# Kernel optimization log

Measured on AMD Instinct MI355X. Metric: run time of the kernel, lower is better.

The kernel has to match this reference:

```python
import jax, jax.numpy as jnp
import numpy as np

NUM_HEADS = 16
MASK_NEG = -66504.0  # matches IPEX causal mask fill value


def setup_inputs() -> dict:
    key = jax.random.key(0)
    ks = jax.random.split(key, 5)
    B, S, E = 1, 2048, 2048
    return {
        "hidden_states": jax.random.normal(ks[0], (B, S, E), dtype=jnp.float32),
        "q_wei": jax.random.normal(ks[1], (E, E), dtype=jnp.float32) * (E ** -0.5),
        "k_wei": jax.random.normal(ks[2], (E, E), dtype=jnp.float32) * (E ** -0.5),
        "v_wei": jax.random.normal(ks[3], (E, E), dtype=jnp.float32) * (E ** -0.5),
        "out_wei": jax.random.normal(ks[4], (E, E), dtype=jnp.float32) * (E ** -0.5),
    }


def reference(hidden_states, q_wei, k_wei, v_wei, out_wei):
    B, S, E = hidden_states.shape
    H = NUM_HEADS
    D = E // H
    # qkv_normal (row-major path): x @ W, [B,S,E]
    q = hidden_states @ q_wei
    k = hidden_states @ k_wei
    v = hidden_states @ v_wei
    # compute_qkv view + normal_combine permute -> [B,H,S,D]
    q = q.reshape(B, S, H, D).transpose(0, 2, 1, 3)
    k = k.reshape(B, S, H, D).transpose(0, 2, 1, 3)
    v = v.reshape(B, S, H, D).transpose(0, 2, 1, 3)
    # naive_self_attention: scores, causal mask add, THEN scale divide
    scores = jnp.einsum("bhqd,bhkd->bhqk", q, k)  # [B,H,S,S]
    causal = jnp.triu(jnp.full((S, S), MASK_NEG, dtype=scores.dtype), k=1)
    scores = scores + causal[None, None]
    scores = scores / jnp.sqrt(jnp.asarray(D, dtype=scores.dtype))
    probs = jax.nn.softmax(scores.astype(jnp.float32), axis=-1).astype(q.dtype)
    attn = jnp.einsum("bhqk,bhkd->bhqd", probs, v)  # [B,H,S,D]
    # merge heads and output projection
    attn = attn.transpose(0, 2, 1, 3).reshape(B, S, E)
    return attn @ out_wei
```

## Files before the change

kernel.cpp:

```cpp
#include <hip/hip_runtime.h>

#define F16 _Float16
typedef __attribute__((ext_vector_type(8))) _Float16 half8;
typedef __attribute__((ext_vector_type(4))) float f32x4;

constexpr int S = 2048;
constexpr int E = 2048;
constexpr float MASK_NEG = -66504.0f;
constexpr float INV_SQRT_D = 0.08838834764831845f;
constexpr float MASK_SC = MASK_NEG * INV_SQRT_D;

__device__ __forceinline__ void gload16(const void* g, void* l) {
  __builtin_amdgcn_global_load_lds((const __attribute__((address_space(1))) void*)g,
                                   (__attribute__((address_space(3))) void*)l, 16, 0, 0);
}

__global__ __launch_bounds__(256) void cast_f32_f16_k(const float* __restrict__ x,
                                                      F16* __restrict__ y) {
  size_t i = ((size_t)blockIdx.x * 256 + threadIdx.x) * 8;
  float4 a = *(const float4*)(x + i);
  float4 b = *(const float4*)(x + i + 4);
  half8 h;
  h[0] = (F16)a.x; h[1] = (F16)a.y; h[2] = (F16)a.z; h[3] = (F16)a.w;
  h[4] = (F16)b.x; h[5] = (F16)b.y; h[6] = (F16)b.z; h[7] = (F16)b.w;
  *(half8*)(y + i) = h;
}

__global__ __launch_bounds__(256) void transpose_cast2_k(const float* __restrict__ W0,
                                                         const float* __restrict__ W1,
                                                         F16* __restrict__ D0,
                                                         F16* __restrict__ D1) {
  const float* W = blockIdx.z ? W1 : W0;
  F16* Wt = blockIdx.z ? D1 : D0;
  __shared__ float tile[64][65];
  const int t = threadIdx.x;
  const int bx = blockIdx.x, by = blockIdx.y;
  {
    int r = t >> 4, c = (t & 15) << 2;
    const float* src = W + (size_t)(by * 64 + r) * E + bx * 64 + c;
    #pragma unroll
    for (int i = 0; i < 4; ++i) {
      float4 v = *(const float4*)(src + (size_t)i * 16 * E);
      tile[r + i * 16][c + 0] = v.x; tile[r + i * 16][c + 1] = v.y;
      tile[r + i * 16][c + 2] = v.z; tile[r + i * 16][c + 3] = v.w;
    }
  }
  __syncthreads();
  {
    int r = t >> 2, c = (t & 3) << 4;
    half8 v0, v1;
    #pragma unroll
    for (int i = 0; i < 8; ++i) v0[i] = (F16)tile[c + i][r];
    #pragma unroll
    for (int i = 0; i < 8; ++i) v1[i] = (F16)tile[c + 8 + i][r];
    F16* dst = Wt + (size_t)(bx * 64 + r) * E + by * 64 + c;
    *(half8*)dst = v0;
    *(half8*)(dst + 8) = v1;
  }
}

template <int MODE>
__global__ __launch_bounds__(256, 2) void gemm_bt_k(const F16* __restrict__ A,
                                                    const F16* __restrict__ Bt,
                                                    void* __restrict__ C0v,
                                                    void* __restrict__ C1v) {
  constexpr int K = 2048, N = 2048;
  __shared__ F16 sA[128 * 64];
  __shared__ F16 sB[128 * 64];
  const int t = threadIdx.x;
  const int lane = t & 63, wave = t >> 6;
  const int wr = wave >> 1, wc = wave & 1;
  const int bm = blockIdx.y, bn = blockIdx.x;

  f32x4 acc[4][4];
  #pragma unroll
  for (int mi = 0; mi < 4; ++mi)
    #pragma unroll
    for (int ni = 0; ni < 4; ++ni) acc[mi][ni] = (f32x4){0.f, 0.f, 0.f, 0.f};

  const int rb = t >> 3;
  const int bofs = (t & 7) << 4;
  const int kOff = (bofs ^ ((rb & 7) << 4)) >> 1;
  const F16* aSrc = A + (size_t)(bm * 128 + rb) * K + kOff;
  const F16* bSrc = Bt + (size_t)(bn * 128 + rb) * K + kOff;
  F16* aDst = sA + t * 8;
  F16* bDst = sB + t * 8;

  for (int bk = 0; bk < K; bk += 64) {
    #pragma unroll
    for (int it = 0; it < 4; ++it) {
      gload16(aSrc + (size_t)it * 32 * K + bk, aDst + it * 2048);
      gload16(bSrc + (size_t)it * 32 * K + bk, bDst + it * 2048);
    }
    __syncthreads();
    #pragma unroll
    for (int kk = 0; kk < 2; ++kk) {
      half8 af[4], bf[4];
      const int kb = kk * 64 + ((lane >> 4) << 4);
      #pragma unroll
      for (int i = 0; i < 4; ++i) {
        const int ra = wr * 64 + i * 16 + (lane & 15);
        af[i] = *(const half8*)((const char*)sA + ra * 128 + (kb ^ ((ra & 7) << 4)));
        const int rn = wc * 64 + i * 16 + (lane & 15);
        bf[i] = *(const half8*)((const char*)sB + rn * 128 + (kb ^ ((rn & 7) << 4)));
      }
      #pragma unroll
      for (int mi = 0; mi < 4; ++mi)
        #pragma unroll
        for (int ni = 0; ni < 4; ++ni)
          acc[mi][ni] = __builtin_amdgcn_mfma_f32_16x16x32_f16(af[mi], bf[ni], acc[mi][ni], 0, 0, 0);
    }
    __syncthreads();
  }

  const float scale = (MODE == 1 && bn < 16) ? INV_SQRT_D : 1.0f;
  void* Cv = (MODE == 1 && bn >= 16) ? C1v : C0v;
  const int cb = (MODE == 1 ? (bn & 15) : bn) * 128;

  #pragma unroll
  for (int mi = 0; mi < 4; ++mi) {
    const int r0 = bm * 128 + wr * 64 + mi * 16 + ((lane >> 4) << 2);
    #pragma unroll
    for (int ni = 0; ni < 4; ++ni) {
      const int c = cb + wc * 64 + ni * 16 + (lane & 15);
      #pragma unroll
      for (int j = 0; j < 4; ++j) {
        if (MODE == 2)
          ((float*)Cv)[(size_t)(r0 + j) * N + c] = acc[mi][ni][j];
        else
          ((F16*)Cv)[(size_t)(r0 + j) * N + c] = (F16)(acc[mi][ni][j] * scale);
      }
    }
  }
}

__global__ __launch_bounds__(256, 2) void attn_fwd_k(const F16* __restrict__ Q,
                                                     const F16* __restrict__ Km,
                                                     const F16* __restrict__ Vt,
                                                     F16* __restrict__ O) {
  __shared__ F16 sK[2][64 * 128];
  __shared__ F16 sV[2][128 * 64];
  __shared__ F16 sP[64 * 64];
  const int t = threadIdx.x, lane = t & 63, w = t >> 6;
  const int h = blockIdx.x & 15, qt = 31 - (blockIdx.x >> 4);
  const int qrow0 = qt * 64 + w * 16;

  half8 qf[4];
  {
    const int r = qrow0 + (lane & 15);
    const F16* qp = Q + (size_t)r * E + h * 128 + ((lane >> 4) << 3);
    #pragma unroll
    for (int kd = 0; kd < 4; ++kd) qf[kd] = *(const half8*)(qp + kd * 32);
  }

  f32x4 oacc[8];
  #pragma unroll
  for (int i = 0; i < 8; ++i) oacc[i] = (f32x4){0.f, 0.f, 0.f, 0.f};
  float mrow[4] = {-3e38f, -3e38f, -3e38f, -3e38f};
  float lrow[4] = {0.f, 0.f, 0.f, 0.f};

  const int rk = t >> 4;
  const int kcol = (((t & 15) << 4) ^ ((rk & 15) << 4)) >> 1;
  const int rv = t >> 3;
  const int vcol = (((t & 7) << 4) ^ ((rv & 7) << 4)) >> 1;
  const F16* kBase = Km + (size_t)rk * E + h * 128 + kcol;
  const F16* vBase = Vt + (size_t)(h * 128 + rv) * S + vcol;

  auto stage = [&](int kt, int b) {
    const F16* kSrc = kBase + (size_t)kt * 64 * E;
    const F16* vSrc = vBase + kt * 64;
    #pragma unroll
    for (int it = 0; it < 4; ++it) {
      gload16(kSrc + (size_t)it * 16 * E, &sK[b][t * 8 + it * 2048]);
      gload16(vSrc + (size_t)it * 32 * S, &sV[b][t * 8 + it * 2048]);
    }
  };

  stage(0, 0);

  for (int kt = 0; kt <= qt; ++kt) {
    __syncthreads();
    if (kt < qt) stage(kt + 1, (kt + 1) & 1);
    const char* bK = (const char*)sK[kt & 1];
    const char* bV = (const char*)sV[kt & 1];

    f32x4 sacc[4];
    #pragma unroll
    for (int i = 0; i < 4; ++i) sacc[i] = (f32x4){0.f, 0.f, 0.f, 0.f};
    #pragma unroll
    for (int kd = 0; kd < 4; ++kd) {
      const int kb = kd * 64 + ((lane >> 4) << 4);
      #pragma unroll
      for (int ni = 0; ni < 4; ++ni) {
        const int rn = ni * 16 + (lane & 15);
        half8 bf = *(const half8*)(bK + rn * 256 + (kb ^ ((rn & 15) << 4)));
        sacc[ni] = __builtin_amdgcn_mfma_f32_16x16x32_f16(qf[kd], bf, sacc[ni], 0, 0, 0);
      }
    }

    const bool diag = (kt == qt);
    float pvv[4][4];
    const int qg0 = qrow0 + ((lane >> 4) << 2);
    const int kg0 = kt * 64 + (lane & 15);
    #pragma unroll
    for (int j = 0; j < 4; ++j) {
      float mx = -3e38f;
      #pragma unroll
      for (int ni = 0; ni < 4; ++ni) {
        float s = sacc[ni][j];
        if (diag && (kg0 + ni * 16) > (qg0 + j)) s += MASK_SC;
        pvv[ni][j] = s;
        mx = fmaxf(mx, s);
      }
      mx = fmaxf(mx, __shfl_xor(mx, 1));
      mx = fmaxf(mx, __shfl_xor(mx, 2));
      mx = fmaxf(mx, __shfl_xor(mx, 4));
      mx = fmaxf(mx, __shfl_xor(mx, 8));
      const float mnew = fmaxf(mrow[j], mx);
      const float sc = __expf(mrow[j] - mnew);
      float rs = 0.f;
      #pragma unroll
      for (int ni = 0; ni < 4; ++ni) {
        const float p = __expf(pvv[ni][j] - mnew);
        pvv[ni][j] = p;
        rs += p;
      }
      rs += __shfl_xor(rs, 1);
      rs += __shfl_xor(rs, 2);
      rs += __shfl_xor(rs, 4);
      rs += __shfl_xor(rs, 8);
      lrow[j] = lrow[j] * sc + rs;
      mrow[j] = mnew;
      #pragma unroll
      for (int df = 0; df < 8; ++df) oacc[df][j] *= sc;
    }

    {
      const int rl0 = w * 16 + ((lane >> 4) << 2);
      #pragma unroll
      for (int ni = 0; ni < 4; ++ni) {
        const int cb = (ni * 16 + (lane & 15)) * 2;
        #pragma unroll
        for (int j = 0; j < 4; ++j) {
          const int r = rl0 + j;
          *(F16*)((char*)sP + r * 128 + (cb ^ ((r & 7) << 4))) = (F16)pvv[ni][j];
        }
      }
    }

    #pragma unroll
    for (int kk = 0; kk < 2; ++kk) {
      const int kb = kk * 64 + ((lane >> 4) << 4);
      const int ra = w * 16 + (lane & 15);
      half8 pa = *(const half8*)((const char*)sP + ra * 128 + (kb ^ ((ra & 7) << 4)));
      #pragma unroll
      for (int df = 0; df < 8; ++df) {
        const int rd = df * 16 + (lane & 15);
        half8 vf = *(const half8*)(bV + rd * 128 + (kb ^ ((rd & 7) << 4)));
        oacc[df] = __builtin_amdgcn_mfma_f32_16x16x32_f16(pa, vf, oacc[df], 0, 0, 0);
      }
    }
  }

  #pragma unroll
  for (int j = 0; j < 4; ++j) {
    const float inv = 1.0f / lrow[j];
    const int r = qrow0 + ((lane >> 4) << 2) + j;
    F16* op = O + (size_t)r * E + h * 128 + (lane & 15);
    #pragma unroll
    for (int df = 0; df < 8; ++df) op[df * 16] = (F16)(oacc[df][j] * inv);
  }
}

extern "C" void kernel_launch(void* const* d_in, const int* in_sizes, int n_in,
                              void* d_out, int out_size, void* d_ws, size_t ws_size,
                              hipStream_t stream) {
  const float* X  = (const float*)d_in[0];
  const float* Wq = (const float*)d_in[1];
  const float* Wk = (const float*)d_in[2];
  const float* Wv = (const float*)d_in[3];
  const float* Wo = (const float*)d_in[4];
  float* out = (float*)d_out;

  const size_t MAT = (size_t)2048 * 2048;
  F16* Xh  = (F16*)d_ws;
  F16* Wt0 = Xh + MAT;
  F16* Wt1 = Wt0 + MAT;
  F16* Qh  = Wt1 + MAT;
  F16* Kh  = Qh + MAT;
  F16* Vh  = Kh + MAT;

  dim3 b256(256);
  cast_f32_f16_k<<<dim3(MAT / 2048), b256, 0, stream>>>(X, Xh);

  transpose_cast2_k<<<dim3(32, 32, 2), b256, 0, stream>>>(Wq, Wk, Wt0, Wt1);
  gemm_bt_k<1><<<dim3(32, 16), b256, 0, stream>>>(Xh, Wt0, Qh, Kh);

  transpose_cast2_k<<<dim3(32, 32, 2), b256, 0, stream>>>(Wv, Wo, Wt0, Wt1);
  gemm_bt_k<0><<<dim3(16, 16), b256, 0, stream>>>(Wt0, Xh, Vh, nullptr);

  attn_fwd_k<<<dim3(512), b256, 0, stream>>>(Qh, Kh, Vh, Xh);

  gemm_bt_k<2><<<dim3(16, 16), b256, 0, stream>>>(Xh, Wt1, out, nullptr);
}
```

Measured before the change: 196.2 us.

## Shrink GEMM M-tile, per-wave P buffers, lazy softmax rescale, priority hints in attention

The GEMM tile height drops from 128 to 64 rows, doubling grid size so the 256-CU part gets more blocks for the 2048x2048 projections, at the cost of lower arithmetic intensity per block. The attention kernel interleaves long and short causal query tiles in block order, gives each wave a private P buffer, and raises wave priority around the MFMA sections. It also skips the running-max rescale of the output accumulator unless a row's max grows by more than a threshold of 8. That trades exact max tracking for fewer exponentials and multiplies, accepting larger but bounded exponent values.

```diff
diff --git a/kernel.cpp b/kernel.cpp
--- a/kernel.cpp
+++ b/kernel.cpp
@@ -65,47 +65,51 @@
                                                     void* __restrict__ C0v,
                                                     void* __restrict__ C1v) {
   constexpr int K = 2048, N = 2048;
-  __shared__ F16 sA[128 * 64];
+  __shared__ F16 sA[64 * 64];
   __shared__ F16 sB[128 * 64];
   const int t = threadIdx.x;
   const int lane = t & 63, wave = t >> 6;
   const int wr = wave >> 1, wc = wave & 1;
   const int bm = blockIdx.y, bn = blockIdx.x;
 
-  f32x4 acc[4][4];
+  f32x4 acc[2][4];
   #pragma unroll
-  for (int mi = 0; mi < 4; ++mi)
+  for (int mi = 0; mi < 2; ++mi)
     #pragma unroll
     for (int ni = 0; ni < 4; ++ni) acc[mi][ni] = (f32x4){0.f, 0.f, 0.f, 0.f};
 
   const int rb = t >> 3;
   const int bofs = (t & 7) << 4;
   const int kOff = (bofs ^ ((rb & 7) << 4)) >> 1;
-  const F16* aSrc = A + (size_t)(bm * 128 + rb) * K + kOff;
+  const F16* aSrc = A + (size_t)(bm * 64 + rb) * K + kOff;
   const F16* bSrc = Bt + (size_t)(bn * 128 + rb) * K + kOff;
   F16* aDst = sA + t * 8;
   F16* bDst = sB + t * 8;
 
   for (int bk = 0; bk < K; bk += 64) {
     #pragma unroll
-    for (int it = 0; it < 4; ++it) {
+    for (int it = 0; it < 2; ++it)
       gload16(aSrc + (size_t)it * 32 * K + bk, aDst + it * 2048);
+    #pragma unroll
+    for (int it = 0; it < 4; ++it)
       gload16(bSrc + (size_t)it * 32 * K + bk, bDst + it * 2048);
-    }
     __syncthreads();
     #pragma unroll
     for (int kk = 0; kk < 2; ++kk) {
-      half8 af[4], bf[4];
+      half8 af[2], bf[4];
       const int kb = kk * 64 + ((lane >> 4) << 4);
       #pragma unroll
+      for (int i = 0; i < 2; ++i) {
+        const int ra = wr * 32 + i * 16 + (lane & 15);
+        af[i] = *(const half8*)((const char*)sA + ra * 128 + (kb ^ ((ra & 7) << 4)));
+      }
+      #pragma unroll
       for (int i = 0; i < 4; ++i) {
-        const int ra = wr * 64 + i * 16 + (lane & 15);
-        af[i] = *(const half8*)((const char*)sA + ra * 128 + (kb ^ ((ra & 7) << 4)));
         const int rn = wc * 64 + i * 16 + (lane & 15);
         bf[i] = *(const half8*)((const char*)sB + rn * 128 + (kb ^ ((rn & 7) << 4)));
       }
       #pragma unroll
-      for (int mi = 0; mi < 4; ++mi)
+      for (int mi = 0; mi < 2; ++mi)
         #pragma unroll
         for (int ni = 0; ni < 4; ++ni)
           acc[mi][ni] = __builtin_amdgcn_mfma_f32_16x16x32_f16(af[mi], bf[ni], acc[mi][ni], 0, 0, 0);
@@ -118,8 +122,8 @@
   const int cb = (MODE == 1 ? (bn & 15) : bn) * 128;
 
   #pragma unroll
-  for (int mi = 0; mi < 4; ++mi) {
-    const int r0 = bm * 128 + wr * 64 + mi * 16 + ((lane >> 4) << 2);
+  for (int mi = 0; mi < 2; ++mi) {
+    const int r0 = bm * 64 + wr * 32 + mi * 16 + ((lane >> 4) << 2);
     #pragma unroll
     for (int ni = 0; ni < 4; ++ni) {
       const int c = cb + wc * 64 + ni * 16 + (lane & 15);
@@ -140,9 +144,11 @@
                                                      F16* __restrict__ O) {
   __shared__ F16 sK[2][64 * 128];
   __shared__ F16 sV[2][128 * 64];
-  __shared__ F16 sP[64 * 64];
+  __shared__ F16 sP[4][16 * 64];
   const int t = threadIdx.x, lane = t & 63, w = t >> 6;
-  const int h = blockIdx.x & 15, qt = 31 - (blockIdx.x >> 4);
+  const int h = blockIdx.x & 15;
+  const int bq = blockIdx.x >> 4;
+  const int qt = (bq < 16) ? (31 - bq) : (bq - 16);
   const int qrow0 = qt * 64 + w * 16;
 
   half8 qf[4];
@@ -165,6 +171,7 @@
   const int vcol = (((t & 7) << 4) ^ ((rv & 7) << 4)) >> 1;
   const F16* kBase = Km + (size_t)rk * E + h * 128 + kcol;
   const F16* vBase = Vt + (size_t)(h * 128 + rv) * S + vcol;
+  F16* myP = (F16*)sP[w];
 
   auto stage = [&](int kt, int b) {
     const F16* kSrc = kBase + (size_t)kt * 64 * E;
@@ -177,16 +184,18 @@
   };
 
   stage(0, 0);
-
-  for (int kt = 0; kt <= qt; ++kt) {
+  const int nt = qt + 1;
+
+  for (int kt = 0; kt < nt; ++kt) {
     __syncthreads();
-    if (kt < qt) stage(kt + 1, (kt + 1) & 1);
+    if (kt + 1 < nt) stage(kt + 1, (kt + 1) & 1);
     const char* bK = (const char*)sK[kt & 1];
     const char* bV = (const char*)sV[kt & 1];
 
     f32x4 sacc[4];
     #pragma unroll
     for (int i = 0; i < 4; ++i) sacc[i] = (f32x4){0.f, 0.f, 0.f, 0.f};
+    __builtin_amdgcn_s_setprio(1);
     #pragma unroll
     for (int kd = 0; kd < 4; ++kd) {
       const int kb = kd * 64 + ((lane >> 4) << 4);
@@ -197,11 +206,13 @@
         sacc[ni] = __builtin_amdgcn_mfma_f32_16x16x32_f16(qf[kd], bf, sacc[ni], 0, 0, 0);
       }
     }
-
-    const bool diag = (kt == qt);
-    float pvv[4][4];
+    __builtin_amdgcn_s_setprio(0);
+
+    const bool diag = (kt == nt - 1);
     const int qg0 = qrow0 + ((lane >> 4) << 2);
     const int kg0 = kt * 64 + (lane & 15);
+    float mxs[4];
+    bool need = false;
     #pragma unroll
     for (int j = 0; j < 4; ++j) {
       float mx = -3e38f;
@@ -209,50 +220,74 @@
       for (int ni = 0; ni < 4; ++ni) {
         float s = sacc[ni][j];
         if (diag && (kg0 + ni * 16) > (qg0 + j)) s += MASK_SC;
-        pvv[ni][j] = s;
+        sacc[ni][j] = s;
         mx = fmaxf(mx, s);
       }
       mx = fmaxf(mx, __shfl_xor(mx, 1));
       mx = fmaxf(mx, __shfl_xor(mx, 2));
       mx = fmaxf(mx, __shfl_xor(mx, 4));
       mx = fmaxf(mx, __shfl_xor(mx, 8));
-      const float mnew = fmaxf(mrow[j], mx);
-      const float sc = __expf(mrow[j] - mnew);
-      float rs = 0.f;
-      #pragma unroll
-      for (int ni = 0; ni < 4; ++ni) {
-        const float p = __expf(pvv[ni][j] - mnew);
-        pvv[ni][j] = p;
-        rs += p;
-      }
-      rs += __shfl_xor(rs, 1);
-      rs += __shfl_xor(rs, 2);
-      rs += __shfl_xor(rs, 4);
-      rs += __shfl_xor(rs, 8);
-      lrow[j] = lrow[j] * sc + rs;
-      mrow[j] = mnew;
-      #pragma unroll
-      for (int df = 0; df < 8; ++df) oacc[df][j] *= sc;
+      mxs[j] = mx;
+      need = need || (mx > mrow[j] + 8.0f);
+    }
+    if (__any(need)) {
+      #pragma unroll
+      for (int j = 0; j < 4; ++j) {
+        const float mnew = fmaxf(mrow[j], mxs[j]);
+        const float sc = __expf(mrow[j] - mnew);
+        float rs = 0.f;
+        #pragma unroll
+        for (int ni = 0; ni < 4; ++ni) {
+          const float p = __expf(sacc[ni][j] - mnew);
+          sacc[ni][j] = p;
+          rs += p;
+        }
+        rs += __shfl_xor(rs, 1);
+        rs += __shfl_xor(rs, 2);
+        rs += __shfl_xor(rs, 4);
+        rs += __shfl_xor(rs, 8);
+        lrow[j] = lrow[j] * sc + rs;
+        mrow[j] = mnew;
+        #pragma unroll
+        for (int df = 0; df < 8; ++df) oacc[df][j] *= sc;
+      }
+    } else {
+      #pragma unroll
+      for (int j = 0; j < 4; ++j) {
+        float rs = 0.f;
+        #pragma unroll
+        for (int ni = 0; ni < 4; ++ni) {
+          const float p = __expf(sacc[ni][j] - mrow[j]);
+          sacc[ni][j] = p;
+          rs += p;
+        }
+        rs += __shfl_xor(rs, 1);
+        rs += __shfl_xor(rs, 2);
+        rs += __shfl_xor(rs, 4);
+        rs += __shfl_xor(rs, 8);
+        lrow[j] += rs;
+      }
     }
 
     {
-      const int rl0 = w * 16 + ((lane >> 4) << 2);
+      const int rl0 = (lane >> 4) << 2;
       #pragma unroll
       for (int ni = 0; ni < 4; ++ni) {
         const int cb = (ni * 16 + (lane & 15)) * 2;
         #pragma unroll
         for (int j = 0; j < 4; ++j) {
           const int r = rl0 + j;
-          *(F16*)((char*)sP + r * 128 + (cb ^ ((r & 7) << 4))) = (F16)pvv[ni][j];
+          *(F16*)((char*)myP + r * 128 + (cb ^ ((r & 7) << 4))) = (F16)sacc[ni][j];
         }
       }
     }
 
+    __builtin_amdgcn_s_setprio(1);
     #pragma unroll
     for (int kk = 0; kk < 2; ++kk) {
       const int kb = kk * 64 + ((lane >> 4) << 4);
-      const int ra = w * 16 + (lane & 15);
-      half8 pa = *(const half8*)((const char*)sP + ra * 128 + (kb ^ ((ra & 7) << 4)));
+      const int ra = lane & 15;
+      half8 pa = *(const half8*)((const char*)myP + ra * 128 + (kb ^ ((ra & 7) << 4)));
       #pragma unroll
       for (int df = 0; df < 8; ++df) {
         const int rd = df * 16 + (lane & 15);
@@ -260,6 +295,7 @@
         oacc[df] = __builtin_amdgcn_mfma_f32_16x16x32_f16(pa, vf, oacc[df], 0, 0, 0);
       }
     }
+    __builtin_amdgcn_s_setprio(0);
   }
 
   #pragma unroll
@@ -294,12 +330,12 @@
   cast_f32_f16_k<<<dim3(MAT / 2048), b256, 0, stream>>>(X, Xh);
 
   transpose_cast2_k<<<dim3(32, 32, 2), b256, 0, stream>>>(Wq, Wk, Wt0, Wt1);
-  gemm_bt_k<1><<<dim3(32, 16), b256, 0, stream>>>(Xh, Wt0, Qh, Kh);
+  gemm_bt_k<1><<<dim3(32, 32), b256, 0, stream>>>(Xh, Wt0, Qh, Kh);
 
   transpose_cast2_k<<<dim3(32, 32, 2), b256, 0, stream>>>(Wv, Wo, Wt0, Wt1);
-  gemm_bt_k<0><<<dim3(16, 16), b256, 0, stream>>>(Wt0, Xh, Vh, nullptr);
+  gemm_bt_k<0><<<dim3(16, 32), b256, 0, stream>>>(Wt0, Xh, Vh, nullptr);
 
   attn_fwd_k<<<dim3(512), b256, 0, stream>>>(Qh, Kh, Vh, Xh);
 
-  gemm_bt_k<2><<<dim3(16, 16), b256, 0, stream>>>(Xh, Wt1, out, nullptr);
-}
+  gemm_bt_k<2><<<dim3(16, 32), b256, 0, stream>>>(Xh, Wt1, out, nullptr);
+}
```

Result: no change. 195.1 us (-0.6%).
